# Optimization experiments

Measured on AMD Instinct MI355X. Metric: run time of the kernel, lower is better.

## Reference

```python
import jax, jax.numpy as jnp
import numpy as np

N, E, T = 6144, 98304, 32
D_IN, D, D_FF, H, OUT = 128, 256, 256, 4, 2
DH = D // H
EPS = 1e-5


def setup_inputs() -> dict:
    key = jax.random.key(0)
    ks = jax.random.split(key, 24)
    s = 0.05
    inp = {
        "x": jax.random.normal(ks[0], (N, D_IN), jnp.float32),
        "edge_index": jax.random.randint(ks[1], (2, E), 0, N, jnp.int64 if jax.config.jax_enable_x64 else jnp.int32),
        "timesteps": jnp.sort(jax.random.randint(ks[2], (N,), 0, T)),
        "lin_l_w": jax.random.normal(ks[3], (D, D_IN), jnp.float32) * s,
        "lin_l_b": jnp.zeros((D,), jnp.float32),
        "lin_r_w": jax.random.normal(ks[4], (D, D_IN), jnp.float32) * s,
        "bn_gamma": jnp.ones((D,), jnp.float32),
        "bn_beta": jnp.zeros((D,), jnp.float32),
        "in_proj_w": jax.random.normal(ks[5], (2, 3 * D, D), jnp.float32) * s,
        "in_proj_b": jnp.zeros((2, 3 * D), jnp.float32),
        "out_w": jax.random.normal(ks[6], (2, D, D), jnp.float32) * s,
        "out_b": jnp.zeros((2, D), jnp.float32),
        "ff1_w": jax.random.normal(ks[7], (2, D_FF, D), jnp.float32) * s,
        "ff1_b": jnp.zeros((2, D_FF), jnp.float32),
        "ff2_w": jax.random.normal(ks[8], (2, D, D_FF), jnp.float32) * s,
        "ff2_b": jnp.zeros((2, D), jnp.float32),
        "ln1_g": jnp.ones((2, D), jnp.float32),
        "ln1_b": jnp.zeros((2, D), jnp.float32),
        "ln2_g": jnp.ones((2, D), jnp.float32),
        "ln2_b": jnp.zeros((2, D), jnp.float32),
        "cls_w": jax.random.normal(ks[9], (OUT, D), jnp.float32) * s,
        "cls_b": jnp.zeros((OUT,), jnp.float32),
    }
    return inp


def _layernorm(h, g, b):
    mu = jnp.mean(h, -1, keepdims=True)
    v = jnp.var(h, -1, keepdims=True)
    return (h - mu) * jax.lax.rsqrt(v + EPS) * g + b


def _forward(x, edge_index, timesteps, lin_l_w, lin_l_b, lin_r_w, bn_gamma, bn_beta,
             in_proj_w, in_proj_b, out_w, out_b, ff1_w, ff1_b, ff2_w, ff2_b,
             ln1_g, ln1_b, ln2_g, ln2_b, cls_w, cls_b):
    # SAGEConv (mean aggregation): out = lin_l(mean_{j->i} x_j) + lin_r(x_i)
    src, dst = edge_index[0], edge_index[1]
    agg = jax.ops.segment_sum(x[src], dst, num_segments=N)
    cnt = jax.ops.segment_sum(jnp.ones((E,), x.dtype), dst, num_segments=N)
    agg = agg / jnp.maximum(cnt, 1.0)[:, None]
    h = agg @ lin_l_w.T + lin_l_b + x @ lin_r_w.T

    # BatchNorm1d (training batch stats) + ReLU
    mu = jnp.mean(h, 0)
    var = jnp.var(h, 0)
    h = (h - mu) * jax.lax.rsqrt(var + EPS) * bn_gamma + bn_beta
    h = jax.nn.relu(h)

    # Per-timestep transformer == full attention with block-diagonal mask
    mask = timesteps[:, None] == timesteps[None, :]  # [N, N]
    neg = jnp.finfo(h.dtype).min

    for l in range(2):
        # self-attention (post-norm TransformerEncoderLayer)
        qkv = h @ in_proj_w[l].T + in_proj_b[l]             # [N, 3D]
        q, k, v = jnp.split(qkv, 3, axis=-1)
        q = q.reshape(N, H, DH).transpose(1, 0, 2)          # [H, N, DH]
        k = k.reshape(N, H, DH).transpose(1, 0, 2)
        v = v.reshape(N, H, DH).transpose(1, 0, 2)
        scores = jnp.einsum('hnd,hmd->hnm', q, k) / jnp.sqrt(jnp.asarray(DH, h.dtype))
        scores = jnp.where(mask[None], scores, neg)
        attn = jax.nn.softmax(scores, axis=-1)
        o = jnp.einsum('hnm,hmd->hnd', attn, v).transpose(1, 0, 2).reshape(N, D)
        o = o @ out_w[l].T + out_b[l]
        h = _layernorm(h + o, ln1_g[l], ln1_b[l])
        # FFN
        f = jax.nn.relu(h @ ff1_w[l].T + ff1_b[l]) @ ff2_w[l].T + ff2_b[l]
        h = _layernorm(h + f, ln2_g[l], ln2_b[l])

    return h @ cls_w.T + cls_b  # [N, OUT]


def reference(x, edge_index, timesteps, lin_l_w, lin_l_b, lin_r_w, bn_gamma, bn_beta,
              in_proj_w, in_proj_b, out_w, out_b, ff1_w, ff1_b, ff2_w, ff2_b,
              ln1_g, ln1_b, ln2_g, ln2_b, cls_w, cls_b):
    return _forward(x, edge_index, timesteps, lin_l_w, lin_l_b, lin_r_w, bn_gamma, bn_beta,
                    in_proj_w, in_proj_b, out_w, out_b, ff1_w, ff1_b, ff2_w, ff2_b,
                    ln1_g, ln1_b, ln2_g, ln2_b, cls_w, cls_b)
```

## Files before the change

### kernel.cpp

```cpp
#include <hip/hip_runtime.h>

#define NN   6144
#define EE   98304
#define DIN  128
#define DD   256
#define TT   32
#define NH   4
#define ATTN_Z 6

typedef __attribute__((ext_vector_type(8))) short short8;
typedef __attribute__((ext_vector_type(4))) float f32x4;

__device__ __forceinline__ unsigned short f2bf(float f) {
    unsigned u = __float_as_uint(f);
    return (unsigned short)((u + 0x7fffu + ((u >> 16) & 1u)) >> 16);
}
__device__ __forceinline__ unsigned pk2(float a, float b) {
    return (unsigned)f2bf(a) | ((unsigned)f2bf(b) << 16);
}
__device__ __forceinline__ short8 pack8(float4 a, float4 b, float s) {
    union { unsigned u[4]; short8 v; } r;
    r.u[0] = pk2(a.x * s, a.y * s);
    r.u[1] = pk2(a.z * s, a.w * s);
    r.u[2] = pk2(b.x * s, b.y * s);
    r.u[3] = pk2(b.z * s, b.w * s);
    return r.v;
}

__global__ void aml_hist_k(const int* __restrict__ ei, int* __restrict__ deg) {
    int e = blockIdx.x * 256 + threadIdx.x;
    if (e < EE) atomicAdd(&deg[ei[EE + e]], 1);
}

__global__ void aml_scan_k(const int* __restrict__ deg, int* __restrict__ rowptr,
                           int* __restrict__ cursor) {
    int t = threadIdx.x;
    int base = t * 24;
    int loc[24];
    int s = 0;
    #pragma unroll
    for (int j = 0; j < 24; ++j) { loc[j] = s; s += deg[base + j]; }
    __shared__ int part[256];
    part[t] = s;
    __syncthreads();
    for (int o = 1; o < 256; o <<= 1) {
        int v = (t >= o) ? part[t - o] : 0;
        __syncthreads();
        part[t] += v;
        __syncthreads();
    }
    int off = (t > 0) ? part[t - 1] : 0;
    #pragma unroll
    for (int j = 0; j < 24; ++j) {
        rowptr[base + j] = off + loc[j];
        cursor[base + j] = off + loc[j];
    }
    if (t == 255) rowptr[NN] = part[255];
}

__global__ void aml_scatter2_k(const int* __restrict__ ei, int* __restrict__ cursor,
                               int* __restrict__ eid) {
    int e = blockIdx.x * 256 + threadIdx.x;
    if (e >= EE) return;
    int slot = atomicAdd(&cursor[ei[EE + e]], 1);
    eid[slot] = ei[e];
}

__global__ void aml_gather_k(const float* __restrict__ x, const int* __restrict__ rowptr,
                             const int* __restrict__ eid, float* __restrict__ ac) {
    int node = blockIdx.x * 4 + (threadIdx.x >> 6);
    int lane = threadIdx.x & 63;
    int p0 = rowptr[node], p1 = rowptr[node + 1];
    float ax = 0.f, ay = 0.f;
    int j = p0;
    for (; j + 1 < p1; j += 2) {
        int s0 = eid[j], s1 = eid[j + 1];
        float2 v0 = *(const float2*)(x + (size_t)s0 * DIN + lane * 2);
        float2 v1 = *(const float2*)(x + (size_t)s1 * DIN + lane * 2);
        ax += v0.x + v1.x; ay += v0.y + v1.y;
    }
    if (j < p1) {
        float2 v = *(const float2*)(x + (size_t)eid[j] * DIN + lane * 2);
        ax += v.x; ay += v.y;
    }
    float inv = 1.0f / fmaxf((float)(p1 - p0), 1.0f);
    float2 xr = *(const float2*)(x + (size_t)node * DIN + lane * 2);
    float2 mv = { ax * inv, ay * inv };
    *(float2*)(ac + (size_t)node * DD + lane * 2) = mv;
    *(float2*)(ac + (size_t)node * DD + DIN + lane * 2) = xr;
}

__global__ void aml_wcat_k(const float* __restrict__ wl, const float* __restrict__ wr,
                           float* __restrict__ wcat) {
    int d = blockIdx.x;
    int k = threadIdx.x;
    wcat[(size_t)d * DD + k] = (k < DIN) ? wl[(size_t)d * DIN + k]
                                         : wr[(size_t)d * DIN + (k - DIN)];
}

template <int RELU>
__global__ __launch_bounds__(256)
void aml_gemm_k(const float* __restrict__ A, const float* __restrict__ W,
                const float* __restrict__ bias, float* __restrict__ C, int M) {
    __shared__ __align__(16) unsigned char lds[65536];
    const int t = threadIdx.x;
    const int brow = blockIdx.x * 64;
    const int bcol = blockIdx.y * 64;

    const float* srcA = A + (size_t)brow * 256;
    const float* srcW = W + (size_t)bcol * 256;
    #pragma unroll
    for (int p = 0; p < 8; ++p) {
        int c = t + p * 256;
        int row = c >> 5;
        int colb = (c & 31) * 16;
        int dst = row * 512 + (colb ^ ((row & 7) << 4));
        const float* sA = srcA + row * 256 + (c & 31) * 8;
        const float* sW = srcW + row * 256 + (c & 31) * 8;
        float4 a0 = *(const float4*)sA;
        float4 a1 = *(const float4*)(sA + 4);
        uint4 pa = { pk2(a0.x, a0.y), pk2(a0.z, a0.w), pk2(a1.x, a1.y), pk2(a1.z, a1.w) };
        *(uint4*)(lds + dst) = pa;
        float4 w0 = *(const float4*)sW;
        float4 w1 = *(const float4*)(sW + 4);
        uint4 pw = { pk2(w0.x, w0.y), pk2(w0.z, w0.w), pk2(w1.x, w1.y), pk2(w1.z, w1.w) };
        *(uint4*)(lds + 32768 + dst) = pw;
    }
    __syncthreads();

    const int wave = t >> 6, lane = t & 63;
    const int lrow = lane & 15, lk = lane >> 4;
    const int arow = wave * 16 + lrow;
    f32x4 acc[4] = {};
    #pragma unroll
    for (int ks = 0; ks < 8; ++ks) {
        int kbyte = ks * 64 + lk * 16;
        short8 af = *(const short8*)(lds + arow * 512 + (kbyte ^ ((arow & 7) << 4)));
        #pragma unroll
        for (int ct = 0; ct < 4; ++ct) {
            int wrow = ct * 16 + lrow;
            short8 bf = *(const short8*)(lds + 32768 + wrow * 512 + (kbyte ^ ((wrow & 7) << 4)));
            acc[ct] = __builtin_amdgcn_mfma_f32_16x16x32_bf16(af, bf, acc[ct], 0, 0, 0);
        }
    }

    #pragma unroll
    for (int ct = 0; ct < 4; ++ct) {
        int col = bcol + ct * 16 + lrow;
        float bv = bias[col];
        #pragma unroll
        for (int r = 0; r < 4; ++r) {
            int grow = brow + wave * 16 + lk * 4 + r;
            float v = acc[ct][r] + bv;
            if (RELU) v = fmaxf(v, 0.0f);
            C[(size_t)grow * M + col] = v;
        }
    }
}

__global__ void aml_bn_stats_k(const float* __restrict__ h, float* __restrict__ stats) {
    int d = threadIdx.x;
    int r0 = blockIdx.x * 96;
    float s = 0.f, ss = 0.f;
    for (int i = 0; i < 96; ++i) {
        float v = h[(size_t)(r0 + i) * DD + d];
        s += v; ss += v * v;
    }
    atomicAdd(&stats[d], s);
    atomicAdd(&stats[DD + d], ss);
}

__global__ void aml_bn_apply_k(float* __restrict__ h, const float* __restrict__ stats,
                               const float* __restrict__ g, const float* __restrict__ b) {
    int idx = blockIdx.x * 256 + threadIdx.x;
    int d = idx & (DD - 1);
    float mu = stats[d] * (1.0f / NN);
    float var = stats[DD + d] * (1.0f / NN) - mu * mu;
    float v = (h[idx] - mu) * rsqrtf(var + 1e-5f) * g[d] + b[d];
    h[idx] = fmaxf(v, 0.0f);
}

__global__ void aml_offsets_k(const int* __restrict__ ts, int* __restrict__ offs) {
    int t = threadIdx.x;
    if (t > TT) return;
    int lo = 0, hi = NN;
    while (lo < hi) {
        int mid = (lo + hi) >> 1;
        if (ts[mid] < t) lo = mid + 1; else hi = mid;
    }
    offs[t] = lo;
}

__global__ __launch_bounds__(256)
void aml_attn_k(const float* __restrict__ qkv, const int* __restrict__ offs,
                float* __restrict__ o) {
    int tb = blockIdx.x, head = blockIdx.y, z = blockIdx.z;
    int start = offs[tb], end = offs[tb + 1];
    int S = end - start;
    if (S <= z * 64) return;
    int t = threadIdx.x, wave = t >> 6, lane = t & 63;
    int lq = lane & 15, lk = lane >> 4;
    int qoff = head * 64;

    __shared__ __align__(16) unsigned char Kl[8192];
    __shared__ __align__(16) unsigned char Vt[8192];
    __shared__ __align__(16) unsigned char Pl[4][2048];
    __shared__ float Ol[4][16][65];

    int qi = start + z * 64 + wave * 16 + lq;
    int qic = min(qi, end - 1);
    const float* qp = qkv + (size_t)qic * 768 + qoff + lk * 8;
    short8 qf[2];
    #pragma unroll
    for (int ks = 0; ks < 2; ++ks) {
        float4 a = *(const float4*)(qp + ks * 32);
        float4 b = *(const float4*)(qp + ks * 32 + 4);
        qf[ks] = pack8(a, b, 0.125f);
    }

    float m = -1e30f, l = 0.f;
    f32x4 acc[4] = {};

    int ntile = (S + 63) >> 6;
    for (int tile = 0; tile < ntile; ++tile) {
        int jcnt = S - tile * 64; if (jcnt > 64) jcnt = 64;
        {
            int j = t >> 2, d0 = (t & 3) * 16;
            unsigned char* krow = Kl + j * 128;
            if (j < jcnt) {
                const float* kp = qkv + (size_t)(start + tile * 64 + j) * 768 + 256 + qoff + d0;
                float4 k0 = *(const float4*)kp, k1 = *(const float4*)(kp + 4);
                float4 k2 = *(const float4*)(kp + 8), k3 = *(const float4*)(kp + 12);
                uint4 pc0 = { pk2(k0.x, k0.y), pk2(k0.z, k0.w), pk2(k1.x, k1.y), pk2(k1.z, k1.w) };
                uint4 pc1 = { pk2(k2.x, k2.y), pk2(k2.z, k2.w), pk2(k3.x, k3.y), pk2(k3.z, k3.w) };
                *(uint4*)(krow + ((d0 * 2) ^ ((j & 7) << 4))) = pc0;
                *(uint4*)(krow + ((d0 * 2 + 16) ^ ((j & 7) << 4))) = pc1;
                const float* vp = kp + 256;
                float4 v0 = *(const float4*)vp, v1 = *(const float4*)(vp + 4);
                float4 v2 = *(const float4*)(vp + 8), v3 = *(const float4*)(vp + 12);
                float vv[16] = { v0.x, v0.y, v0.z, v0.w, v1.x, v1.y, v1.z, v1.w,
                                 v2.x, v2.y, v2.z, v2.w, v3.x, v3.y, v3.z, v3.w };
                #pragma unroll
                for (int i = 0; i < 16; ++i) {
                    int d = d0 + i;
                    *(unsigned short*)(Vt + d * 128 + ((j * 2) ^ ((d & 7) << 4))) = f2bf(vv[i]);
                }
            } else {
                uint4 zz = { 0, 0, 0, 0 };
                *(uint4*)(krow + ((d0 * 2) ^ ((j & 7) << 4))) = zz;
                *(uint4*)(krow + ((d0 * 2 + 16) ^ ((j & 7) << 4))) = zz;
                #pragma unroll
                for (int i = 0; i < 16; ++i) {
                    int d = d0 + i;
                    *(unsigned short*)(Vt + d * 128 + ((j * 2) ^ ((d & 7) << 4))) = 0;
                }
            }
        }
        __syncthreads();

        f32x4 sv[4];
        #pragma unroll
        for (int kt = 0; kt < 4; ++kt) {
            int kr = kt * 16 + lq;
            f32x4 s = {};
            #pragma unroll
            for (int ks = 0; ks < 2; ++ks) {
                short8 kf = *(const short8*)(Kl + kr * 128 + ((ks * 64 + lk * 16) ^ ((kr & 7) << 4)));
                s = __builtin_amdgcn_mfma_f32_16x16x32_bf16(kf, qf[ks], s, 0, 0, 0);
            }
            sv[kt] = s;
        }
        float pm = -1e30f;
        #pragma unroll
        for (int kt = 0; kt < 4; ++kt) {
            #pragma unroll
            for (int r = 0; r < 4; ++r) {
                int kk = tile * 64 + kt * 16 + lk * 4 + r;
                float s = (kk < S) ? sv[kt][r] : -1e30f;
                sv[kt][r] = s;
                pm = fmaxf(pm, s);
            }
        }
        pm = fmaxf(pm, __shfl_xor(pm, 16));
        pm = fmaxf(pm, __shfl_xor(pm, 32));
        float mn = fmaxf(m, pm);
        float corr = __expf(m - mn);
        m = mn;
        float ps = 0.f;
        #pragma unroll
        for (int kt = 0; kt < 4; ++kt) {
            #pragma unroll
            for (int r = 0; r < 4; ++r) {
                float p = __expf(sv[kt][r] - mn);
                sv[kt][r] = p;
                ps += p;
            }
            uint2 w = { pk2(sv[kt][0], sv[kt][1]), pk2(sv[kt][2], sv[kt][3]) };
            *(uint2*)(Pl[wave] + lq * 128 + ((kt * 32 + lk * 8) ^ ((lq & 7) << 4))) = w;
        }
        ps += __shfl_xor(ps, 16);
        ps += __shfl_xor(ps, 32);
        l = l * corr + ps;
        #pragma unroll
        for (int dt = 0; dt < 4; ++dt) {
            #pragma unroll
            for (int r = 0; r < 4; ++r) acc[dt][r] *= corr;
        }
        #pragma unroll
        for (int ks = 0; ks < 2; ++ks) {
            short8 pf = *(const short8*)(Pl[wave] + lq * 128 + ((ks * 64 + lk * 16) ^ ((lq & 7) << 4)));
            #pragma unroll
            for (int dt = 0; dt < 4; ++dt) {
                int dr = dt * 16 + lq;
                short8 vf = *(const short8*)(Vt + dr * 128 + ((ks * 64 + lk * 16) ^ ((dr & 7) << 4)));
                acc[dt] = __builtin_amdgcn_mfma_f32_16x16x32_bf16(vf, pf, acc[dt], 0, 0, 0);
            }
        }
        __syncthreads();
    }

    float linv = 1.0f / l;
    #pragma unroll
    for (int dt = 0; dt < 4; ++dt) {
        #pragma unroll
        for (int r = 0; r < 4; ++r)
            Ol[wave][lq][dt * 16 + lk * 4 + r] = acc[dt][r] * linv;
    }
    int q2 = lane >> 2, c2 = lane & 3;
    int qg = start + z * 64 + wave * 16 + q2;
    if (qg < end) {
        float* op = o + (size_t)qg * DD + qoff + c2 * 16;
        const float* sp = &Ol[wave][q2][c2 * 16];
        #pragma unroll
        for (int i = 0; i < 4; ++i) ((float4*)op)[i] = *(const float4*)(sp + i * 4);
    }
}

__global__ void aml_ln_k(float* __restrict__ h, const float* __restrict__ r,
                         const float* __restrict__ g, const float* __restrict__ b) {
    int row = blockIdx.x * 4 + (threadIdx.x >> 6);
    int lane = threadIdx.x & 63;
    float* hp = h + (size_t)row * DD + lane * 4;
    float4 v = *(const float4*)hp;
    float4 rv = *(const float4*)(r + (size_t)row * DD + lane * 4);
    v.x += rv.x; v.y += rv.y; v.z += rv.z; v.w += rv.w;
    float s = v.x + v.y + v.z + v.w;
    float ss = v.x * v.x + v.y * v.y + v.z * v.z + v.w * v.w;
    #pragma unroll
    for (int off = 32; off; off >>= 1) {
        s += __shfl_xor(s, off);
        ss += __shfl_xor(ss, off);
    }
    float mu = s * (1.0f / DD);
    float var = ss * (1.0f / DD) - mu * mu;
    float inv = rsqrtf(var + 1e-5f);
    float4 gv = *(const float4*)(g + lane * 4);
    float4 bv = *(const float4*)(b + lane * 4);
    v.x = (v.x - mu) * inv * gv.x + bv.x;
    v.y = (v.y - mu) * inv * gv.y + bv.y;
    v.z = (v.z - mu) * inv * gv.z + bv.z;
    v.w = (v.w - mu) * inv * gv.w + bv.w;
    *(float4*)hp = v;
}

__global__ void aml_cls_k(const float* __restrict__ h, const float* __restrict__ w,
                          const float* __restrict__ b, float* __restrict__ out) {
    int row = blockIdx.x * 4 + (threadIdx.x >> 6);
    int lane = threadIdx.x & 63;
    float4 v = *(const float4*)(h + (size_t)row * DD + lane * 4);
    float4 w0 = *(const float4*)(w + lane * 4);
    float4 w1 = *(const float4*)(w + DD + lane * 4);
    float a0 = v.x * w0.x + v.y * w0.y + v.z * w0.z + v.w * w0.w;
    float a1 = v.x * w1.x + v.y * w1.y + v.z * w1.z + v.w * w1.w;
    #pragma unroll
    for (int off = 32; off; off >>= 1) {
        a0 += __shfl_xor(a0, off);
        a1 += __shfl_xor(a1, off);
    }
    if (lane == 0) {
        out[row * 2]     = a0 + b[0];
        out[row * 2 + 1] = a1 + b[1];
    }
}

extern "C" void kernel_launch(void* const* d_in, const int* in_sizes, int n_in,
                              void* d_out, int out_size, void* d_ws, size_t ws_size,
                              hipStream_t stream) {
    const float* x       = (const float*)d_in[0];
    const int*   ei      = (const int*)d_in[1];
    const int*   ts      = (const int*)d_in[2];
    const float* lin_l_w = (const float*)d_in[3];
    const float* lin_l_b = (const float*)d_in[4];
    const float* lin_r_w = (const float*)d_in[5];
    const float* bn_g    = (const float*)d_in[6];
    const float* bn_b    = (const float*)d_in[7];
    const float* inp_w   = (const float*)d_in[8];
    const float* inp_b   = (const float*)d_in[9];
    const float* out_w   = (const float*)d_in[10];
    const float* out_b   = (const float*)d_in[11];
    const float* ff1_w   = (const float*)d_in[12];
    const float* ff1_b   = (const float*)d_in[13];
    const float* ff2_w   = (const float*)d_in[14];
    const float* ff2_b   = (const float*)d_in[15];
    const float* ln1_g   = (const float*)d_in[16];
    const float* ln1_b   = (const float*)d_in[17];
    const float* ln2_g   = (const float*)d_in[18];
    const float* ln2_b   = (const float*)d_in[19];
    const float* cls_w   = (const float*)d_in[20];
    const float* cls_b   = (const float*)d_in[21];

    float* ws     = (float*)d_ws;
    float* stats  = ws;
    int*   deg    = (int*)(stats + 512);
    int*   rowptr = deg + NN;
    int*   cursor = rowptr + NN + 1;
    int*   eid    = cursor + NN;
    int*   offs   = eid + EE;
    float* h      = (float*)(offs + 64);
    float* qkv    = h + (size_t)NN * DD;
    float* t1     = qkv + (size_t)NN * 768;
    float* t2     = t1 + (size_t)NN * DD;
    float* ac     = qkv;
    float* wcat   = t1;

    hipMemsetAsync(stats, 0, 512 * sizeof(float) + NN * sizeof(int), stream);

    aml_hist_k<<<EE / 256, 256, 0, stream>>>(ei, deg);
    aml_scan_k<<<1, 256, 0, stream>>>(deg, rowptr, cursor);
    aml_scatter2_k<<<EE / 256, 256, 0, stream>>>(ei, cursor, eid);
    aml_gather_k<<<NN / 4, 256, 0, stream>>>(x, rowptr, eid, ac);
    aml_wcat_k<<<DD, 256, 0, stream>>>(lin_l_w, lin_r_w, wcat);
    aml_offsets_k<<<1, 64, 0, stream>>>(ts, offs);
    aml_gemm_k<0><<<dim3(NN / 64, 4), 256, 0, stream>>>(ac, wcat, lin_l_b, h, DD);
    aml_bn_stats_k<<<64, 256, 0, stream>>>(h, stats);
    aml_bn_apply_k<<<(NN * DD) / 256, 256, 0, stream>>>(h, stats, bn_g, bn_b);

    for (int l = 0; l < 2; ++l) {
        aml_gemm_k<0><<<dim3(NN / 64, 12), 256, 0, stream>>>(h, inp_w + (size_t)l * 768 * DD,
                                                             inp_b + (size_t)l * 768, qkv, 768);
        aml_attn_k<<<dim3(TT, NH, ATTN_Z), 256, 0, stream>>>(qkv, offs, t1);
        aml_gemm_k<0><<<dim3(NN / 64, 4), 256, 0, stream>>>(t1, out_w + (size_t)l * DD * DD,
                                                            out_b + (size_t)l * DD, t2, DD);
        aml_ln_k<<<NN / 4, 256, 0, stream>>>(h, t2, ln1_g + (size_t)l * DD, ln1_b + (size_t)l * DD);
        aml_gemm_k<1><<<dim3(NN / 64, 4), 256, 0, stream>>>(h, ff1_w + (size_t)l * DD * DD,
                                                            ff1_b + (size_t)l * DD, t1, DD);
        aml_gemm_k<0><<<dim3(NN / 64, 4), 256, 0, stream>>>(t1, ff2_w + (size_t)l * DD * DD,
                                                            ff2_b + (size_t)l * DD, t2, DD);
        aml_ln_k<<<NN / 4, 256, 0, stream>>>(h, t2, ln2_g + (size_t)l * DD, ln2_b + (size_t)l * DD);
    }

    aml_cls_k<<<NN / 4, 256, 0, stream>>>(h, cls_w, cls_b, (float*)d_out);
}
```

Measured before the change: 183.5 us.

## Pre-convert weights to bf16 once and fuse residual+LayerNorm into GEMM epilogue

All linear weights are converted to bf16 in one prep kernel, which also computes the timestep offsets. The GEMM is rewritten as a single-wave kernel: each wave covers 16 rows by 256 columns, reads bf16 weights straight from global memory with no LDS staging, and converts A to bf16 on the fly. The out-proj and FF2 GEMMs now fuse the residual add and LayerNorm into the epilogue, removing the separate LN kernels and the t2 buffer. The trade-off is more global and L2 traffic for weights, since LDS reuse is gone, and much smaller blocks.

```diff
diff --git a/kernel.cpp b/kernel.cpp
--- a/kernel.cpp
+++ b/kernel.cpp
@@ -7,6 +7,7 @@
 #define TT   32
 #define NH   4
 #define ATTN_Z 6
+#define WROWS 3328
 
 typedef __attribute__((ext_vector_type(8))) short short8;
 typedef __attribute__((ext_vector_type(4))) float f32x4;
@@ -90,70 +91,115 @@
     *(float2*)(ac + (size_t)node * DD + DIN + lane * 2) = xr;
 }
 
-__global__ void aml_wcat_k(const float* __restrict__ wl, const float* __restrict__ wr,
-                           float* __restrict__ wcat) {
-    int d = blockIdx.x;
+__global__ void aml_prep_k(const float* __restrict__ lin_l_w, const float* __restrict__ lin_r_w,
+                           const float* __restrict__ inp_w, const float* __restrict__ out_w,
+                           const float* __restrict__ ff1_w, const float* __restrict__ ff2_w,
+                           const int* __restrict__ ts, unsigned short* __restrict__ wb,
+                           int* __restrict__ offs) {
+    int r = blockIdx.x;
+    if (r == WROWS) {
+        int t = threadIdx.x;
+        if (t <= TT) {
+            int lo = 0, hi = NN;
+            while (lo < hi) { int mid = (lo + hi) >> 1; if (ts[mid] < t) lo = mid + 1; else hi = mid; }
+            offs[t] = lo;
+        }
+        return;
+    }
     int k = threadIdx.x;
-    wcat[(size_t)d * DD + k] = (k < DIN) ? wl[(size_t)d * DIN + k]
-                                         : wr[(size_t)d * DIN + (k - DIN)];
-}
-
-template <int RELU>
-__global__ __launch_bounds__(256)
-void aml_gemm_k(const float* __restrict__ A, const float* __restrict__ W,
-                const float* __restrict__ bias, float* __restrict__ C, int M) {
-    __shared__ __align__(16) unsigned char lds[65536];
-    const int t = threadIdx.x;
-    const int brow = blockIdx.x * 64;
-    const int bcol = blockIdx.y * 64;
-
-    const float* srcA = A + (size_t)brow * 256;
-    const float* srcW = W + (size_t)bcol * 256;
-    #pragma unroll
-    for (int p = 0; p < 8; ++p) {
-        int c = t + p * 256;
-        int row = c >> 5;
-        int colb = (c & 31) * 16;
-        int dst = row * 512 + (colb ^ ((row & 7) << 4));
-        const float* sA = srcA + row * 256 + (c & 31) * 8;
-        const float* sW = srcW + row * 256 + (c & 31) * 8;
-        float4 a0 = *(const float4*)sA;
-        float4 a1 = *(const float4*)(sA + 4);
-        uint4 pa = { pk2(a0.x, a0.y), pk2(a0.z, a0.w), pk2(a1.x, a1.y), pk2(a1.z, a1.w) };
-        *(uint4*)(lds + dst) = pa;
-        float4 w0 = *(const float4*)sW;
-        float4 w1 = *(const float4*)(sW + 4);
-        uint4 pw = { pk2(w0.x, w0.y), pk2(w0.z, w0.w), pk2(w1.x, w1.y), pk2(w1.z, w1.w) };
-        *(uint4*)(lds + 32768 + dst) = pw;
-    }
-    __syncthreads();
-
-    const int wave = t >> 6, lane = t & 63;
+    float v;
+    if (r < 256) {
+        v = (k < DIN) ? lin_l_w[r * DIN + k] : lin_r_w[r * DIN + (k - DIN)];
+    } else {
+        int r2 = r - 256;
+        int l = r2 / 1536, r3 = r2 % 1536;
+        const float* src; int rr;
+        if (r3 < 768)       { src = inp_w + (size_t)l * 768 * DD; rr = r3; }
+        else if (r3 < 1024) { src = out_w + (size_t)l * DD * DD;  rr = r3 - 768; }
+        else if (r3 < 1280) { src = ff1_w + (size_t)l * DD * DD;  rr = r3 - 1024; }
+        else                { src = ff2_w + (size_t)l * DD * DD;  rr = r3 - 1280; }
+        v = src[(size_t)rr * DD + k];
+    }
+    wb[(size_t)r * DD + k] = f2bf(v);
+}
+
+template <int MODE>
+__global__ __launch_bounds__(64)
+void aml_gemm2_k(const float* __restrict__ A, const unsigned short* __restrict__ Wb,
+                 const float* __restrict__ bias, float* __restrict__ C, int Mout,
+                 const float* __restrict__ g, const float* __restrict__ bv) {
+    const int lane = threadIdx.x;
     const int lrow = lane & 15, lk = lane >> 4;
-    const int arow = wave * 16 + lrow;
-    f32x4 acc[4] = {};
+    const int row0 = blockIdx.x * 16;
+    const int colb = blockIdx.y * 256;
+    const float* ap = A + (size_t)(row0 + lrow) * 256;
+
+    f32x4 acc[16] = {};
     #pragma unroll
     for (int ks = 0; ks < 8; ++ks) {
-        int kbyte = ks * 64 + lk * 16;
-        short8 af = *(const short8*)(lds + arow * 512 + (kbyte ^ ((arow & 7) << 4)));
-        #pragma unroll
-        for (int ct = 0; ct < 4; ++ct) {
-            int wrow = ct * 16 + lrow;
-            short8 bf = *(const short8*)(lds + 32768 + wrow * 512 + (kbyte ^ ((wrow & 7) << 4)));
+        int k0 = ks * 32 + lk * 8;
+        float4 a0 = *(const float4*)(ap + k0);
+        float4 a1 = *(const float4*)(ap + k0 + 4);
+        short8 af = pack8(a0, a1, 1.0f);
+        #pragma unroll
+        for (int ct = 0; ct < 16; ++ct) {
+            int wrow = colb + ct * 16 + lrow;
+            short8 bf = *(const short8*)(Wb + (size_t)wrow * 256 + k0);
             acc[ct] = __builtin_amdgcn_mfma_f32_16x16x32_bf16(af, bf, acc[ct], 0, 0, 0);
         }
     }
 
-    #pragma unroll
-    for (int ct = 0; ct < 4; ++ct) {
-        int col = bcol + ct * 16 + lrow;
-        float bv = bias[col];
+    if (MODE < 2) {
+        #pragma unroll
+        for (int ct = 0; ct < 16; ++ct) {
+            int col = colb + ct * 16 + lrow;
+            float bvv = bias[col];
+            #pragma unroll
+            for (int r = 0; r < 4; ++r) {
+                int grow = row0 + lk * 4 + r;
+                float v = acc[ct][r] + bvv;
+                if (MODE == 1) v = fmaxf(v, 0.0f);
+                C[(size_t)grow * Mout + col] = v;
+            }
+        }
+    } else {
+        float s[4] = {}, q[4] = {};
+        #pragma unroll
+        for (int ct = 0; ct < 16; ++ct) {
+            int col = colb + ct * 16 + lrow;
+            float bvv = bias[col];
+            #pragma unroll
+            for (int r = 0; r < 4; ++r) {
+                int grow = row0 + lk * 4 + r;
+                float v = acc[ct][r] + bvv + C[(size_t)grow * 256 + col];
+                acc[ct][r] = v;
+                s[r] += v;
+                q[r] += v * v;
+            }
+        }
+        #pragma unroll
+        for (int off = 1; off < 16; off <<= 1) {
+            #pragma unroll
+            for (int r = 0; r < 4; ++r) {
+                s[r] += __shfl_xor(s[r], off);
+                q[r] += __shfl_xor(q[r], off);
+            }
+        }
+        float mu[4], iv[4];
         #pragma unroll
         for (int r = 0; r < 4; ++r) {
-            int grow = brow + wave * 16 + lk * 4 + r;
-            float v = acc[ct][r] + bv;
-            if (RELU) v = fmaxf(v, 0.0f);
-            C[(size_t)grow * M + col] = v;
+            mu[r] = s[r] * (1.0f / 256.0f);
+            iv[r] = rsqrtf(q[r] * (1.0f / 256.0f) - mu[r] * mu[r] + 1e-5f);
+        }
+        #pragma unroll
+        for (int ct = 0; ct < 16; ++ct) {
+            int col = colb + ct * 16 + lrow;
+            float gv = g[col], bb = bv[col];
+            #pragma unroll
+            for (int r = 0; r < 4; ++r) {
+                int grow = row0 + lk * 4 + r;
+                C[(size_t)grow * 256 + col] = (acc[ct][r] - mu[r]) * iv[r] * gv + bb;
+            }
         }
     }
 }
@@ -178,17 +224,6 @@
     float var = stats[DD + d] * (1.0f / NN) - mu * mu;
     float v = (h[idx] - mu) * rsqrtf(var + 1e-5f) * g[d] + b[d];
     h[idx] = fmaxf(v, 0.0f);
-}
-
-__global__ void aml_offsets_k(const int* __restrict__ ts, int* __restrict__ offs) {
-    int t = threadIdx.x;
-    if (t > TT) return;
-    int lo = 0, hi = NN;
-    while (lo < hi) {
-        int mid = (lo + hi) >> 1;
-        if (ts[mid] < t) lo = mid + 1; else hi = mid;
-    }
-    offs[t] = lo;
 }
 
 __global__ __launch_bounds__(256)
@@ -336,33 +371,6 @@
     }
 }
 
-__global__ void aml_ln_k(float* __restrict__ h, const float* __restrict__ r,
-                         const float* __restrict__ g, const float* __restrict__ b) {
-    int row = blockIdx.x * 4 + (threadIdx.x >> 6);
-    int lane = threadIdx.x & 63;
-    float* hp = h + (size_t)row * DD + lane * 4;
-    float4 v = *(const float4*)hp;
-    float4 rv = *(const float4*)(r + (size_t)row * DD + lane * 4);
-    v.x += rv.x; v.y += rv.y; v.z += rv.z; v.w += rv.w;
-    float s = v.x + v.y + v.z + v.w;
-    float ss = v.x * v.x + v.y * v.y + v.z * v.z + v.w * v.w;
-    #pragma unroll
-    for (int off = 32; off; off >>= 1) {
-        s += __shfl_xor(s, off);
-        ss += __shfl_xor(ss, off);
-    }
-    float mu = s * (1.0f / DD);
-    float var = ss * (1.0f / DD) - mu * mu;
-    float inv = rsqrtf(var + 1e-5f);
-    float4 gv = *(const float4*)(g + lane * 4);
-    float4 bv = *(const float4*)(b + lane * 4);
-    v.x = (v.x - mu) * inv * gv.x + bv.x;
-    v.y = (v.y - mu) * inv * gv.y + bv.y;
-    v.z = (v.z - mu) * inv * gv.z + bv.z;
-    v.w = (v.w - mu) * inv * gv.w + bv.w;
-    *(float4*)hp = v;
-}
-
 __global__ void aml_cls_k(const float* __restrict__ h, const float* __restrict__ w,
                           const float* __restrict__ b, float* __restrict__ out) {
     int row = blockIdx.x * 4 + (threadIdx.x >> 6);
@@ -413,15 +421,24 @@
     float* stats  = ws;
     int*   deg    = (int*)(stats + 512);
     int*   rowptr = deg + NN;
-    int*   cursor = rowptr + NN + 1;
+    int*   cursor = rowptr + NN + 4;
     int*   eid    = cursor + NN;
     int*   offs   = eid + EE;
-    float* h      = (float*)(offs + 64);
+    unsigned short* wb = (unsigned short*)(offs + 64);
+    float* h      = (float*)(wb + (size_t)WROWS * 256);
     float* qkv    = h + (size_t)NN * DD;
     float* t1     = qkv + (size_t)NN * 768;
-    float* t2     = t1 + (size_t)NN * DD;
     float* ac     = qkv;
-    float* wcat   = t1;
+
+    const unsigned short* wb_cat = wb;
+    const unsigned short* wb_inp[2] = { wb + (size_t)(256) * 256,
+                                        wb + (size_t)(256 + 1536) * 256 };
+    const unsigned short* wb_out[2] = { wb + (size_t)(256 + 768) * 256,
+                                        wb + (size_t)(256 + 1536 + 768) * 256 };
+    const unsigned short* wb_ff1[2] = { wb + (size_t)(256 + 1024) * 256,
+                                        wb + (size_t)(256 + 1536 + 1024) * 256 };
+    const unsigned short* wb_ff2[2] = { wb + (size_t)(256 + 1280) * 256,
+                                        wb + (size_t)(256 + 1536 + 1280) * 256 };
 
     hipMemsetAsync(stats, 0, 512 * sizeof(float) + NN * sizeof(int), stream);
 
@@ -429,24 +446,24 @@
     aml_scan_k<<<1, 256, 0, stream>>>(deg, rowptr, cursor);
     aml_scatter2_k<<<EE / 256, 256, 0, stream>>>(ei, cursor, eid);
     aml_gather_k<<<NN / 4, 256, 0, stream>>>(x, rowptr, eid, ac);
-    aml_wcat_k<<<DD, 256, 0, stream>>>(lin_l_w, lin_r_w, wcat);
-    aml_offsets_k<<<1, 64, 0, stream>>>(ts, offs);
-    aml_gemm_k<0><<<dim3(NN / 64, 4), 256, 0, stream>>>(ac, wcat, lin_l_b, h, DD);
+    aml_prep_k<<<WROWS + 1, 256, 0, stream>>>(lin_l_w, lin_r_w, inp_w, out_w, ff1_w, ff2_w,
+                                              ts, wb, offs);
+    aml_gemm2_k<0><<<dim3(NN / 16, 1), 64, 0, stream>>>(ac, wb_cat, lin_l_b, h, DD, nullptr, nullptr);
     aml_bn_stats_k<<<64, 256, 0, stream>>>(h, stats);
     aml_bn_apply_k<<<(NN * DD) / 256, 256, 0, stream>>>(h, stats, bn_g, bn_b);
 
     for (int l = 0; l < 2; ++l) {
-        aml_gemm_k<0><<<dim3(NN / 64, 12), 256, 0, stream>>>(h, inp_w + (size_t)l * 768 * DD,
-                                                             inp_b + (size_t)l * 768, qkv, 768);
+        aml_gemm2_k<0><<<dim3(NN / 16, 3), 64, 0, stream>>>(h, wb_inp[l], inp_b + (size_t)l * 768,
+                                                            qkv, 768, nullptr, nullptr);
         aml_attn_k<<<dim3(TT, NH, ATTN_Z), 256, 0, stream>>>(qkv, offs, t1);
-        aml_gemm_k<0><<<dim3(NN / 64, 4), 256, 0, stream>>>(t1, out_w + (size_t)l * DD * DD,
-                                                            out_b + (size_t)l * DD, t2, DD);
-        aml_ln_k<<<NN / 4, 256, 0, stream>>>(h, t2, ln1_g + (size_t)l * DD, ln1_b + (size_t)l * DD);
-        aml_gemm_k<1><<<dim3(NN / 64, 4), 256, 0, stream>>>(h, ff1_w + (size_t)l * DD * DD,
-                                                            ff1_b + (size_t)l * DD, t1, DD);
-        aml_gemm_k<0><<<dim3(NN / 64, 4), 256, 0, stream>>>(t1, ff2_w + (size_t)l * DD * DD,
-                                                            ff2_b + (size_t)l * DD, t2, DD);
-        aml_ln_k<<<NN / 4, 256, 0, stream>>>(h, t2, ln2_g + (size_t)l * DD, ln2_b + (size_t)l * DD);
+        aml_gemm2_k<2><<<dim3(NN / 16, 1), 64, 0, stream>>>(t1, wb_out[l], out_b + (size_t)l * DD,
+                                                            h, DD, ln1_g + (size_t)l * DD,
+                                                            ln1_b + (size_t)l * DD);
+        aml_gemm2_k<1><<<dim3(NN / 16, 1), 64, 0, stream>>>(h, wb_ff1[l], ff1_b + (size_t)l * DD,
+                                                            t1, DD, nullptr, nullptr);
+        aml_gemm2_k<2><<<dim3(NN / 16, 1), 64, 0, stream>>>(t1, wb_ff2[l], ff2_b + (size_t)l * DD,
+                                                            h, DD, ln2_g + (size_t)l * DD,
+                                                            ln2_b + (size_t)l * DD);
     }
 
     aml_cls_k<<<NN / 4, 256, 0, stream>>>(h, cls_w, cls_b, (float*)d_out);
```

Measured after the change: 317.2 us. 1.73x slower.

## Store intermediates and weights as bf16 to halve memory traffic

Applied to the files above, without the earlier changes.

Pre-converts all layer weights to bf16 once in a merged prep kernel that also computes the timestep offsets. Intermediate activations (gathered features, qkv, attention output, FFN hidden, residual branches) are now stored as bf16, while the residual stream h stays fp32. The goal is to halve global memory traffic and drop the per-tile float-to-bf16 packing in the GEMM and attention kernels. In exchange it adds an extra rounding step on stored activations and moves the attention scale onto the fp32 scores.

```diff
diff --git a/kernel.cpp b/kernel.cpp
--- a/kernel.cpp
+++ b/kernel.cpp
@@ -7,24 +7,21 @@
 #define TT   32
 #define NH   4
 #define ATTN_Z 6
+#define WROWS 3328
 
 typedef __attribute__((ext_vector_type(8))) short short8;
 typedef __attribute__((ext_vector_type(4))) float f32x4;
-
-__device__ __forceinline__ unsigned short f2bf(float f) {
+typedef unsigned short u16;
+
+__device__ __forceinline__ float bf2f(u16 u) {
+    return __uint_as_float(((unsigned)u) << 16);
+}
+__device__ __forceinline__ u16 f2bf(float f) {
     unsigned u = __float_as_uint(f);
-    return (unsigned short)((u + 0x7fffu + ((u >> 16) & 1u)) >> 16);
+    return (u16)((u + 0x7fffu + ((u >> 16) & 1u)) >> 16);
 }
 __device__ __forceinline__ unsigned pk2(float a, float b) {
     return (unsigned)f2bf(a) | ((unsigned)f2bf(b) << 16);
-}
-__device__ __forceinline__ short8 pack8(float4 a, float4 b, float s) {
-    union { unsigned u[4]; short8 v; } r;
-    r.u[0] = pk2(a.x * s, a.y * s);
-    r.u[1] = pk2(a.z * s, a.w * s);
-    r.u[2] = pk2(b.x * s, b.y * s);
-    r.u[3] = pk2(b.z * s, b.w * s);
-    return r.v;
 }
 
 __global__ void aml_hist_k(const int* __restrict__ ei, int* __restrict__ deg) {
@@ -67,7 +64,7 @@
 }
 
 __global__ void aml_gather_k(const float* __restrict__ x, const int* __restrict__ rowptr,
-                             const int* __restrict__ eid, float* __restrict__ ac) {
+                             const int* __restrict__ eid, u16* __restrict__ ac) {
     int node = blockIdx.x * 4 + (threadIdx.x >> 6);
     int lane = threadIdx.x & 63;
     int p0 = rowptr[node], p1 = rowptr[node + 1];
@@ -85,46 +82,69 @@
     }
     float inv = 1.0f / fmaxf((float)(p1 - p0), 1.0f);
     float2 xr = *(const float2*)(x + (size_t)node * DIN + lane * 2);
-    float2 mv = { ax * inv, ay * inv };
-    *(float2*)(ac + (size_t)node * DD + lane * 2) = mv;
-    *(float2*)(ac + (size_t)node * DD + DIN + lane * 2) = xr;
-}
-
-__global__ void aml_wcat_k(const float* __restrict__ wl, const float* __restrict__ wr,
-                           float* __restrict__ wcat) {
-    int d = blockIdx.x;
+    *(unsigned*)(ac + (size_t)node * DD + lane * 2) = pk2(ax * inv, ay * inv);
+    *(unsigned*)(ac + (size_t)node * DD + DIN + lane * 2) = pk2(xr.x, xr.y);
+}
+
+__global__ void aml_prep_k(const float* __restrict__ lin_l_w, const float* __restrict__ lin_r_w,
+                           const float* __restrict__ inp_w, const float* __restrict__ out_w,
+                           const float* __restrict__ ff1_w, const float* __restrict__ ff2_w,
+                           const int* __restrict__ ts, u16* __restrict__ wb,
+                           int* __restrict__ offs) {
+    int r = blockIdx.x;
+    if (r == WROWS) {
+        int t = threadIdx.x;
+        if (t <= TT) {
+            int lo = 0, hi = NN;
+            while (lo < hi) { int mid = (lo + hi) >> 1; if (ts[mid] < t) lo = mid + 1; else hi = mid; }
+            offs[t] = lo;
+        }
+        return;
+    }
     int k = threadIdx.x;
-    wcat[(size_t)d * DD + k] = (k < DIN) ? wl[(size_t)d * DIN + k]
-                                         : wr[(size_t)d * DIN + (k - DIN)];
-}
-
-template <int RELU>
+    float v;
+    if (r < 256) {
+        v = (k < DIN) ? lin_l_w[r * DIN + k] : lin_r_w[r * DIN + (k - DIN)];
+    } else {
+        int r2 = r - 256;
+        int l = r2 / 1536, r3 = r2 % 1536;
+        const float* src; int rr;
+        if (r3 < 768)       { src = inp_w + (size_t)l * 768 * DD; rr = r3; }
+        else if (r3 < 1024) { src = out_w + (size_t)l * DD * DD;  rr = r3 - 768; }
+        else if (r3 < 1280) { src = ff1_w + (size_t)l * DD * DD;  rr = r3 - 1024; }
+        else                { src = ff2_w + (size_t)l * DD * DD;  rr = r3 - 1280; }
+        v = src[(size_t)rr * DD + k];
+    }
+    wb[(size_t)r * DD + k] = f2bf(v);
+}
+
+template <int RELU, int AF32, int CF32>
 __global__ __launch_bounds__(256)
-void aml_gemm_k(const float* __restrict__ A, const float* __restrict__ W,
-                const float* __restrict__ bias, float* __restrict__ C, int M) {
+void aml_gemm_k(const void* __restrict__ A, const u16* __restrict__ Wb,
+                const float* __restrict__ bias, void* __restrict__ C, int M) {
     __shared__ __align__(16) unsigned char lds[65536];
     const int t = threadIdx.x;
     const int brow = blockIdx.x * 64;
     const int bcol = blockIdx.y * 64;
 
-    const float* srcA = A + (size_t)brow * 256;
-    const float* srcW = W + (size_t)bcol * 256;
+    const u16* srcW = Wb + (size_t)bcol * 256;
     #pragma unroll
     for (int p = 0; p < 8; ++p) {
         int c = t + p * 256;
         int row = c >> 5;
         int colb = (c & 31) * 16;
         int dst = row * 512 + (colb ^ ((row & 7) << 4));
-        const float* sA = srcA + row * 256 + (c & 31) * 8;
-        const float* sW = srcW + row * 256 + (c & 31) * 8;
-        float4 a0 = *(const float4*)sA;
-        float4 a1 = *(const float4*)(sA + 4);
-        uint4 pa = { pk2(a0.x, a0.y), pk2(a0.z, a0.w), pk2(a1.x, a1.y), pk2(a1.z, a1.w) };
-        *(uint4*)(lds + dst) = pa;
-        float4 w0 = *(const float4*)sW;
-        float4 w1 = *(const float4*)(sW + 4);
-        uint4 pw = { pk2(w0.x, w0.y), pk2(w0.z, w0.w), pk2(w1.x, w1.y), pk2(w1.z, w1.w) };
-        *(uint4*)(lds + 32768 + dst) = pw;
+        if (AF32) {
+            const float* sA = (const float*)A + (size_t)(brow + row) * 256 + (c & 31) * 8;
+            float4 a0 = *(const float4*)sA;
+            float4 a1 = *(const float4*)(sA + 4);
+            uint4 pa = { pk2(a0.x, a0.y), pk2(a0.z, a0.w), pk2(a1.x, a1.y), pk2(a1.z, a1.w) };
+            *(uint4*)(lds + dst) = pa;
+        } else {
+            const u16* sA = (const u16*)A + (size_t)(brow + row) * 256 + (c & 31) * 8;
+            *(uint4*)(lds + dst) = *(const uint4*)sA;
+        }
+        *(uint4*)(lds + 32768 + dst) = *(const uint4*)(srcW + (size_t)row * 256 + (c & 31) * 8);
     }
     __syncthreads();
 
@@ -153,7 +173,8 @@
             int grow = brow + wave * 16 + lk * 4 + r;
             float v = acc[ct][r] + bv;
             if (RELU) v = fmaxf(v, 0.0f);
-            C[(size_t)grow * M + col] = v;
+            if (CF32) ((float*)C)[(size_t)grow * M + col] = v;
+            else      ((u16*)C)[(size_t)grow * M + col] = f2bf(v);
         }
     }
 }
@@ -180,20 +201,9 @@
     h[idx] = fmaxf(v, 0.0f);
 }
 
-__global__ void aml_offsets_k(const int* __restrict__ ts, int* __restrict__ offs) {
-    int t = threadIdx.x;
-    if (t > TT) return;
-    int lo = 0, hi = NN;
-    while (lo < hi) {
-        int mid = (lo + hi) >> 1;
-        if (ts[mid] < t) lo = mid + 1; else hi = mid;
-    }
-    offs[t] = lo;
-}
-
 __global__ __launch_bounds__(256)
-void aml_attn_k(const float* __restrict__ qkv, const int* __restrict__ offs,
-                float* __restrict__ o) {
+void aml_attn_k(const u16* __restrict__ qkv, const int* __restrict__ offs,
+                u16* __restrict__ o) {
     int tb = blockIdx.x, head = blockIdx.y, z = blockIdx.z;
     int start = offs[tb], end = offs[tb + 1];
     int S = end - start;
@@ -209,14 +219,10 @@
 
     int qi = start + z * 64 + wave * 16 + lq;
     int qic = min(qi, end - 1);
-    const float* qp = qkv + (size_t)qic * 768 + qoff + lk * 8;
+    const u16* qp = qkv + (size_t)qic * 768 + qoff + lk * 8;
     short8 qf[2];
-    #pragma unroll
-    for (int ks = 0; ks < 2; ++ks) {
-        float4 a = *(const float4*)(qp + ks * 32);
-        float4 b = *(const float4*)(qp + ks * 32 + 4);
-        qf[ks] = pack8(a, b, 0.125f);
-    }
+    qf[0] = *(const short8*)qp;
+    qf[1] = *(const short8*)(qp + 32);
 
     float m = -1e30f, l = 0.f;
     f32x4 acc[4] = {};
@@ -228,22 +234,14 @@
             int j = t >> 2, d0 = (t & 3) * 16;
             unsigned char* krow = Kl + j * 128;
             if (j < jcnt) {
-                const float* kp = qkv + (size_t)(start + tile * 64 + j) * 768 + 256 + qoff + d0;
-                float4 k0 = *(const float4*)kp, k1 = *(const float4*)(kp + 4);
-                float4 k2 = *(const float4*)(kp + 8), k3 = *(const float4*)(kp + 12);
-                uint4 pc0 = { pk2(k0.x, k0.y), pk2(k0.z, k0.w), pk2(k1.x, k1.y), pk2(k1.z, k1.w) };
-                uint4 pc1 = { pk2(k2.x, k2.y), pk2(k2.z, k2.w), pk2(k3.x, k3.y), pk2(k3.z, k3.w) };
-                *(uint4*)(krow + ((d0 * 2) ^ ((j & 7) << 4))) = pc0;
-                *(uint4*)(krow + ((d0 * 2 + 16) ^ ((j & 7) << 4))) = pc1;
-                const float* vp = kp + 256;
-                float4 v0 = *(const float4*)vp, v1 = *(const float4*)(vp + 4);
-                float4 v2 = *(const float4*)(vp + 8), v3 = *(const float4*)(vp + 12);
-                float vv[16] = { v0.x, v0.y, v0.z, v0.w, v1.x, v1.y, v1.z, v1.w,
-                                 v2.x, v2.y, v2.z, v2.w, v3.x, v3.y, v3.z, v3.w };
+                const u16* kp = qkv + (size_t)(start + tile * 64 + j) * 768 + 256 + qoff + d0;
+                *(uint4*)(krow + ((d0 * 2) ^ ((j & 7) << 4))) = *(const uint4*)kp;
+                *(uint4*)(krow + ((d0 * 2 + 16) ^ ((j & 7) << 4))) = *(const uint4*)(kp + 8);
+                const u16* vp = kp + 256;
                 #pragma unroll
                 for (int i = 0; i < 16; ++i) {
                     int d = d0 + i;
-                    *(unsigned short*)(Vt + d * 128 + ((j * 2) ^ ((d & 7) << 4))) = f2bf(vv[i]);
+                    *(u16*)(Vt + d * 128 + ((j * 2) ^ ((d & 7) << 4))) = vp[i];
                 }
             } else {
                 uint4 zz = { 0, 0, 0, 0 };
@@ -252,7 +250,7 @@
                 #pragma unroll
                 for (int i = 0; i < 16; ++i) {
                     int d = d0 + i;
-                    *(unsigned short*)(Vt + d * 128 + ((j * 2) ^ ((d & 7) << 4))) = 0;
+                    *(u16*)(Vt + d * 128 + ((j * 2) ^ ((d & 7) << 4))) = 0;
                 }
             }
         }
@@ -276,7 +274,7 @@
             #pragma unroll
             for (int r = 0; r < 4; ++r) {
                 int kk = tile * 64 + kt * 16 + lk * 4 + r;
-                float s = (kk < S) ? sv[kt][r] : -1e30f;
+                float s = (kk < S) ? sv[kt][r] * 0.125f : -1e30f;
                 sv[kt][r] = s;
                 pm = fmaxf(pm, s);
             }
@@ -329,21 +327,25 @@
     int q2 = lane >> 2, c2 = lane & 3;
     int qg = start + z * 64 + wave * 16 + q2;
     if (qg < end) {
-        float* op = o + (size_t)qg * DD + qoff + c2 * 16;
+        u16* op = o + (size_t)qg * DD + qoff + c2 * 16;
         const float* sp = &Ol[wave][q2][c2 * 16];
         #pragma unroll
-        for (int i = 0; i < 4; ++i) ((float4*)op)[i] = *(const float4*)(sp + i * 4);
-    }
-}
-
-__global__ void aml_ln_k(float* __restrict__ h, const float* __restrict__ r,
+        for (int i = 0; i < 8; ++i)
+            ((unsigned*)op)[i] = pk2(sp[2 * i], sp[2 * i + 1]);
+    }
+}
+
+__global__ void aml_ln_k(float* __restrict__ h, const u16* __restrict__ r,
                          const float* __restrict__ g, const float* __restrict__ b) {
     int row = blockIdx.x * 4 + (threadIdx.x >> 6);
     int lane = threadIdx.x & 63;
     float* hp = h + (size_t)row * DD + lane * 4;
     float4 v = *(const float4*)hp;
-    float4 rv = *(const float4*)(r + (size_t)row * DD + lane * 4);
-    v.x += rv.x; v.y += rv.y; v.z += rv.z; v.w += rv.w;
+    uint2 rv = *(const uint2*)(r + (size_t)row * DD + lane * 4);
+    v.x += bf2f((u16)(rv.x & 0xffff));
+    v.y += bf2f((u16)(rv.x >> 16));
+    v.z += bf2f((u16)(rv.y & 0xffff));
+    v.w += bf2f((u16)(rv.y >> 16));
     float s = v.x + v.y + v.z + v.w;
     float ss = v.x * v.x + v.y * v.y + v.z * v.z + v.w * v.w;
     #pragma unroll
@@ -413,15 +415,21 @@
     float* stats  = ws;
     int*   deg    = (int*)(stats + 512);
     int*   rowptr = deg + NN;
-    int*   cursor = rowptr + NN + 1;
+    int*   cursor = rowptr + NN + 4;
     int*   eid    = cursor + NN;
     int*   offs   = eid + EE;
-    float* h      = (float*)(offs + 64);
-    float* qkv    = h + (size_t)NN * DD;
-    float* t1     = qkv + (size_t)NN * 768;
-    float* t2     = t1 + (size_t)NN * DD;
-    float* ac     = qkv;
-    float* wcat   = t1;
+    u16*   wb     = (u16*)(offs + 64);
+    float* h      = (float*)(wb + (size_t)WROWS * 256);
+    u16*   qkv    = (u16*)(h + (size_t)NN * DD);
+    u16*   t1     = qkv + (size_t)NN * 768;
+    u16*   t2     = t1 + (size_t)NN * DD;
+    u16*   ac     = qkv;
+
+    const u16* wb_cat = wb;
+    const u16* wb_inp[2] = { wb + (size_t)(256) * 256,        wb + (size_t)(256 + 1536) * 256 };
+    const u16* wb_out[2] = { wb + (size_t)(256 + 768) * 256,  wb + (size_t)(256 + 1536 + 768) * 256 };
+    const u16* wb_ff1[2] = { wb + (size_t)(256 + 1024) * 256, wb + (size_t)(256 + 1536 + 1024) * 256 };
+    const u16* wb_ff2[2] = { wb + (size_t)(256 + 1280) * 256, wb + (size_t)(256 + 1536 + 1280) * 256 };
 
     hipMemsetAsync(stats, 0, 512 * sizeof(float) + NN * sizeof(int), stream);
 
@@ -429,23 +437,23 @@
     aml_scan_k<<<1, 256, 0, stream>>>(deg, rowptr, cursor);
     aml_scatter2_k<<<EE / 256, 256, 0, stream>>>(ei, cursor, eid);
     aml_gather_k<<<NN / 4, 256, 0, stream>>>(x, rowptr, eid, ac);
-    aml_wcat_k<<<DD, 256, 0, stream>>>(lin_l_w, lin_r_w, wcat);
-    aml_offsets_k<<<1, 64, 0, stream>>>(ts, offs);
-    aml_gemm_k<0><<<dim3(NN / 64, 4), 256, 0, stream>>>(ac, wcat, lin_l_b, h, DD);
+    aml_prep_k<<<WROWS + 1, 256, 0, stream>>>(lin_l_w, lin_r_w, inp_w, out_w, ff1_w, ff2_w,
+                                              ts, wb, offs);
+    aml_gemm_k<0, 0, 1><<<dim3(NN / 64, 4), 256, 0, stream>>>(ac, wb_cat, lin_l_b, h, DD);
     aml_bn_stats_k<<<64, 256, 0, stream>>>(h, stats);
     aml_bn_apply_k<<<(NN * DD) / 256, 256, 0, stream>>>(h, stats, bn_g, bn_b);
 
     for (int l = 0; l < 2; ++l) {
-        aml_gemm_k<0><<<dim3(NN / 64, 12), 256, 0, stream>>>(h, inp_w + (size_t)l * 768 * DD,
-                                                             inp_b + (size_t)l * 768, qkv, 768);
+        aml_gemm_k<0, 1, 0><<<dim3(NN / 64, 12), 256, 0, stream>>>(h, wb_inp[l],
+                                                                   inp_b + (size_t)l * 768, qkv, 768);
         aml_attn_k<<<dim3(TT, NH, ATTN_Z), 256, 0, stream>>>(qkv, offs, t1);
-        aml_gemm_k<0><<<dim3(NN / 64, 4), 256, 0, stream>>>(t1, out_w + (size_t)l * DD * DD,
-                                                            out_b + (size_t)l * DD, t2, DD);
+        aml_gemm_k<0, 0, 0><<<dim3(NN / 64, 4), 256, 0, stream>>>(t1, wb_out[l],
+                                                                  out_b + (size_t)l * DD, t2, DD);
         aml_ln_k<<<NN / 4, 256, 0, stream>>>(h, t2, ln1_g + (size_t)l * DD, ln1_b + (size_t)l * DD);
-        aml_gemm_k<1><<<dim3(NN / 64, 4), 256, 0, stream>>>(h, ff1_w + (size_t)l * DD * DD,
-                                                            ff1_b + (size_t)l * DD, t1, DD);
-        aml_gemm_k<0><<<dim3(NN / 64, 4), 256, 0, stream>>>(t1, ff2_w + (size_t)l * DD * DD,
-                                                            ff2_b + (size_t)l * DD, t2, DD);
+        aml_gemm_k<1, 1, 0><<<dim3(NN / 64, 4), 256, 0, stream>>>(h, wb_ff1[l],
+                                                                  ff1_b + (size_t)l * DD, t1, DD);
+        aml_gemm_k<0, 0, 0><<<dim3(NN / 64, 4), 256, 0, stream>>>(t1, wb_ff2[l],
+                                                                  ff2_b + (size_t)l * DD, t2, DD);
         aml_ln_k<<<NN / 4, 256, 0, stream>>>(h, t2, ln2_g + (size_t)l * DD, ln2_b + (size_t)l * DD);
     }
 
```

Result: faster. 163.6 us (-10.8%).
